# Performance work log

Hardware: AMD Instinct MI355X
Metric: run time of the kernel (lower is better)

The kernel has to match this reference:

```python
import jax, jax.numpy as jnp
import numpy as np

N_WIRES = 16
VAR_DEPTH = 2
BATCH = 16


def _param_sizes():
    sizes = []
    n = N_WIRES
    lay = 0
    while n > 1:
        sizes.append(4 * int(np.ceil(N_WIRES / 2 ** lay)) * VAR_DEPTH)
        n = (n + 1) // 2
        lay += 1
    return sizes  # [128, 64, 32, 16]


def _apply_1q(psi, gate, w):
    # psi: (B, 2, ..., 2); gate: (2,2) complex; wire w lives on axis w+1
    psi = jnp.moveaxis(psi, w + 1, -1)
    psi = jnp.einsum('...j,ij->...i', psi, gate)
    return jnp.moveaxis(psi, -1, w + 1)


def _rx(psi, th, w):
    c = jnp.cos(th / 2).astype(jnp.complex64)
    s = jnp.sin(th / 2).astype(jnp.complex64)
    gate = jnp.stack([jnp.stack([c, -1j * s]), jnp.stack([-1j * s, c])])
    return _apply_1q(psi, gate, w)


def _rz(psi, th, w):
    ph = jnp.exp(0.5j * th * jnp.array([-1.0, 1.0], jnp.float32)).astype(jnp.complex64)
    shape = [1] * psi.ndim
    shape[w + 1] = 2
    return psi * ph.reshape(shape)


def _rzz(psi, th, wa, wb):
    # diag(e^{-i t/2}, e^{i t/2}, e^{i t/2}, e^{-i t/2}) -> sign = -1 if bits equal else +1
    sgn = jnp.array([[-1.0, 1.0], [1.0, -1.0]], jnp.float32)
    ph = jnp.exp(0.5j * th * sgn).astype(jnp.complex64)  # symmetric, transpose-safe
    a, b = min(wa, wb) + 1, max(wa, wb) + 1
    shape = [1] * psi.ndim
    shape[a] = 2
    shape[b] = 2
    return psi * ph.reshape(shape)


def _cnot(psi, c, t):
    p0 = jax.lax.slice_in_dim(psi, 0, 1, axis=c + 1)
    p1 = jax.lax.slice_in_dim(psi, 1, 2, axis=c + 1)
    return jnp.concatenate([p0, jnp.flip(p1, axis=t + 1)], axis=c + 1)


def _conv_layer(psi, params, active):
    n = len(active)
    for d in range(VAR_DEPTH):
        for j in range(n):
            base = 4 * j + d * 4 * n
            psi = _rx(psi, params[base + 0], active[j])
            psi = _rz(psi, params[base + 1], active[j])
            psi = _rx(psi, params[base + 2], active[j])
        for bg in (0, 1):
            for j in range(bg, n, 2):
                jn = (j + 1) % n  # ring coupling (wraps last->first)
                base = 4 * j + d * 4 * n
                psi = _rzz(psi, params[base + 3], active[j], active[jn])
    return psi


def _pool(psi, active):
    for j in range(0, len(active), 2):
        if j + 1 < len(active):
            psi = _cnot(psi, active[j], active[j + 1])
    return psi, active[::2]


def _forward(psi, params_list):
    active = list(range(N_WIRES))
    for p in params_list:
        psi = _conv_layer(psi, p, active)
        if len(active) > 1:
            psi, active = _pool(psi, active)
    w = active[0]  # measure Z on the surviving wire (wire 0)
    prob = psi.real ** 2 + psi.imag ** 2
    axes = tuple(a for a in range(1, psi.ndim) if a != w + 1)
    p2 = prob.sum(axis=axes)  # (B, 2)
    return p2[:, 0] - p2[:, 1]


def setup_inputs() -> dict:
    key = jax.random.key(0)
    ks = jax.random.split(key, 8)
    dim = 2 ** N_WIRES
    x_re = jax.random.normal(ks[0], (BATCH, dim), dtype=jnp.float32)
    x_im = jax.random.normal(ks[1], (BATCH, dim), dtype=jnp.float32)
    nrm = jnp.sqrt(jnp.sum(x_re ** 2 + x_im ** 2, axis=1, keepdims=True))
    x_re = x_re / nrm
    x_im = x_im / nrm
    sizes = _param_sizes()
    two_pi = 2.0 * np.pi
    params = [jax.random.uniform(ks[2 + i], (sizes[i],), dtype=jnp.float32) * two_pi
              for i in range(len(sizes))]
    return {"x_re": x_re, "x_im": x_im,
            "params0": params[0], "params1": params[1],
            "params2": params[2], "params3": params[3]}


def reference(x_re, x_im, params0, params1, params2, params3):
    psi = (x_re + 1j * x_im).astype(jnp.complex64)
    psi = psi.reshape((BATCH,) + (2,) * N_WIRES)
    return _forward(psi, [params0, params1, params2, params3])
```

## Files before the change

### kernel.cpp

```cpp
#include <hip/hip_runtime.h>


#define DEV __device__ __forceinline__
#define TBL(i) (tbl + (i)*8)

__device__ static const unsigned char G_CP[60] = {
  15,14,13,12,11,10,9,8,7,6,5,4,3,2,1,0,
  15,14,13,12,11,10,9,8,7,6,5,4,3,2,1,0,
  15,13,11,9,7,5,3,1,
  15,13,11,9,7,5,3,1,
  15,11,7,3,
  15,11,7,3,
  15,7,
  15,7
};
__device__ static const unsigned char G_CQ[60] = {
  14,13,12,11,10,9,8,7,6,5,4,3,2,1,0,15,
  14,13,12,11,10,9,8,7,6,5,4,3,2,1,0,15,
  13,11,9,7,5,3,1,15,
  13,11,9,7,5,3,1,15,
  11,7,3,15,
  11,7,3,15,
  7,15,
  7,15
};

DEV float2 F2(float x, float y){ float2 r; r.x = x; r.y = y; return r; }
DEV float2 cmulf(float2 a, float2 b){ return F2(a.x*b.x - a.y*b.y, a.x*b.y + a.y*b.x); }
DEV int swz(int j){ return j ^ ((j>>4)&15) ^ ((j>>8)&15); }

template<int A,int B>
DEV int mapj(int t, int s){
  int j = ((s&1)<<A) | (((s>>1)&1)<<B);
  int ti = 0;
  #pragma unroll
  for (int b=0;b<11;b++){
    if (b!=A && b!=B){ j |= ((t>>ti)&1)<<b; ti++; }
  }
  return j;
}

template<int SB>
DEV void gate4(float2* a, const float* __restrict__ g){
  float u00r=g[0],u00i=g[1],u01r=g[2],u01i=g[3],u10r=g[4],u10i=g[5],u11r=g[6],u11i=g[7];
  #pragma unroll
  for (int m=0;m<2;m++){
    int i0 = (SB==0) ? (m<<1) : m;
    int i1 = i0 | (1<<SB);
    float2 x0=a[i0], x1=a[i1];
    a[i0] = F2(u00r*x0.x - u00i*x0.y + u01r*x1.x - u01i*x1.y,
               u00r*x0.y + u00i*x0.x + u01r*x1.y + u01i*x1.x);
    a[i1] = F2(u10r*x0.x - u10i*x0.y + u11r*x1.x - u11i*x1.y,
               u10r*x0.y + u10i*x0.x + u11r*x1.y + u11i*x1.x);
  }
}

template<int C0,int N,unsigned M0,unsigned M1>
DEV void diag4(float2* a, const float* __restrict__ tbl, unsigned Ib){
  const unsigned regmask = M0|M1;
  float2 F0 = F2(1.f, 0.f);
  #pragma unroll
  for (int k=0;k<N;k++){
    const int p = G_CP[C0+k], q = G_CQ[C0+k];
    if ( !(((1u<<p)|(1u<<q)) & regmask) ){
      float c = tbl[480 + 2*(C0+k)], s = tbl[481 + 2*(C0+k)];
      unsigned x = ((Ib>>p) ^ (Ib>>q)) & 1u;
      F0 = cmulf(F0, F2(c, x ? s : -s));
    }
  }
  #pragma unroll
  for (int r=0;r<4;r++){
    unsigned Ir = Ib ^ ((r&1)?M0:0u) ^ ((r&2)?M1:0u);
    float2 ph = F0;
    #pragma unroll
    for (int k=0;k<N;k++){
      const int p = G_CP[C0+k], q = G_CQ[C0+k];
      if ( ((1u<<p)|(1u<<q)) & regmask ){
        float c = tbl[480 + 2*(C0+k)], s = tbl[481 + 2*(C0+k)];
        unsigned x = ((Ir>>p) ^ (Ir>>q)) & 1u;
        ph = cmulf(ph, F2(c, x ? s : -s));
      }
    }
    a[r] = cmulf(a[r], ph);
  }
}

DEV unsigned Ia(int j, int o){ return (unsigned)(j | (o<<11)); }
DEV unsigned Ib2(int j, int o){ return (unsigned)((j&63) | (o<<6) | ((j>>6)<<11)); }
DEV unsigned Ic(int j, int o){
  return (unsigned)( ((j&1)<<1) | (((j>>1)&1)<<3) | (((j>>2)&1)<<5)
       | (((j>>3)&63)<<6) | (((j>>9)&1)<<13) | (((j>>10)&1)<<15)
       | (o&1) | (((o>>1)&1)<<2) | (((o>>2)&1)<<4) | (((o>>3)&1)<<12) | (((o>>4)&1)<<14) );
}
DEV int s2perm(int j){ return j ^ (((j>>8)&1)<<6) ^ (((j>>4)&1)<<2) ^ (((j>>1)&1)<<0); }
DEV int s3perm(int j){ return j ^ (((j>>10)&1)<<8) ^ (((j>>4)&1)<<1); }

__global__ void k_setup(const float* __restrict__ p0, const float* __restrict__ p1,
                        const float* __restrict__ p2, const float* __restrict__ p3,
                        float* __restrict__ tbl, float* __restrict__ out){
  int g = threadIdx.x;
  if (g < 16) out[g] = 0.f;
  if (g >= 60) return;
  int d, j, n; const float* P;
  if (g < 32)      { n=16; d=(g>>4)&1; j=g&15; P=p0; }
  else if (g < 48) { n=8;  d=(g>>3)&1; j=g&7;  P=p1; }
  else if (g < 56) { n=4;  d=(g>>2)&1; j=g&3;  P=p2; }
  else             { n=2;  d=(g>>1)&1; j=g&1;  P=p3; }
  int base = 4*j + 4*n*d;
  double th0 = P[base+0], th1 = P[base+1], th2 = P[base+2], th3 = P[base+3];
  double c0 = cos(th0*0.5), s0 = sin(th0*0.5);
  double ca = cos(th1*0.5), sa = sin(th1*0.5);
  double c2 = cos(th2*0.5), s2 = sin(th2*0.5);
  double B00r =  ca*c0, B00i = -sa*c0;
  double B01r = -sa*s0, B01i = -ca*s0;
  double B10r =  sa*s0, B10i = -ca*s0;
  double B11r =  ca*c0, B11i =  sa*c0;
  float* o = tbl + g*8;
  o[0]=(float)(c2*B00r + s2*B10i); o[1]=(float)(c2*B00i - s2*B10r);
  o[2]=(float)(c2*B01r + s2*B11i); o[3]=(float)(c2*B01i - s2*B11r);
  o[4]=(float)(s2*B00i + c2*B10r); o[5]=(float)(-s2*B00r + c2*B10i);
  o[6]=(float)(s2*B01i + c2*B11r); o[7]=(float)(-s2*B01r + c2*B11i);
  tbl[480 + 2*g] = (float)cos(th3*0.5);
  tbl[481 + 2*g] = (float)sin(th3*0.5);
}

__global__ __launch_bounds__(512, 4)
void k_p1(const float* __restrict__ xre, const float* __restrict__ xim,
          const float* __restrict__ tbl, float2* __restrict__ st){
  const int t = threadIdx.x;
  const int batch = blockIdx.x >> 5, o = blockIdx.x & 31;
  const unsigned hi = ((unsigned)batch<<16) | ((unsigned)o<<11);
  __shared__ float2 lds[2][2048];
  float2 a[4];
  {
    unsigned base = hi | ((unsigned)t<<2);
    float4 re = *(const float4*)(xre + base);
    float4 im = *(const float4*)(xim + base);
    a[0]=F2(re.x,im.x); a[1]=F2(re.y,im.y); a[2]=F2(re.z,im.z); a[3]=F2(re.w,im.w);
  }
  gate4<0>(a, TBL(15)); gate4<1>(a, TBL(14));
  #pragma unroll
  for (int s=0;s<4;s++) lds[0][swz(mapj<0,1>(t,s))] = a[s];
  __syncthreads();
  #pragma unroll
  for (int s=0;s<4;s++) a[s] = lds[0][swz(mapj<2,3>(t,s))];
  gate4<0>(a, TBL(13)); gate4<1>(a, TBL(12));
  #pragma unroll
  for (int s=0;s<4;s++) lds[1][swz(mapj<2,3>(t,s))] = a[s];
  __syncthreads();
  #pragma unroll
  for (int s=0;s<4;s++) a[s] = lds[1][swz(mapj<4,5>(t,s))];
  gate4<0>(a, TBL(11)); gate4<1>(a, TBL(10));
  #pragma unroll
  for (int s=0;s<4;s++) lds[0][swz(mapj<4,5>(t,s))] = a[s];
  __syncthreads();
  #pragma unroll
  for (int s=0;s<4;s++) a[s] = lds[0][swz(mapj<6,7>(t,s))];
  gate4<0>(a, TBL(9)); gate4<1>(a, TBL(8));
  #pragma unroll
  for (int s=0;s<4;s++) lds[1][swz(mapj<6,7>(t,s))] = a[s];
  __syncthreads();
  #pragma unroll
  for (int s=0;s<4;s++) a[s] = lds[1][swz(mapj<8,9>(t,s))];
  gate4<0>(a, TBL(7)); gate4<1>(a, TBL(6));
  #pragma unroll
  for (int s=0;s<4;s++) lds[0][swz(mapj<8,9>(t,s))] = a[s];
  __syncthreads();
  #pragma unroll
  for (int s=0;s<4;s++) a[s] = lds[0][swz(mapj<0,10>(t,s))];
  gate4<1>(a, TBL(5));
  #pragma unroll
  for (int s=0;s<4;s++) st[hi | (unsigned)mapj<0,10>(t,s)] = a[s];
}

__global__ __launch_bounds__(512, 4)
void k_p2(const float* __restrict__ tbl, float2* __restrict__ st){
  const int t = threadIdx.x;
  const int batch = blockIdx.x >> 5, o = blockIdx.x & 31;
  const unsigned bb = (unsigned)batch<<16;
  __shared__ float2 lds[2][2048];
  float2 a[4];
  #pragma unroll
  for (int s=0;s<4;s++) a[s] = st[bb | Ib2(mapj<10,9>(t,s), o)];
  gate4<0>(a, TBL(0)); gate4<1>(a, TBL(1));
  #pragma unroll
  for (int s=0;s<4;s++) lds[0][swz(mapj<10,9>(t,s))] = a[s];
  __syncthreads();
  #pragma unroll
  for (int s=0;s<4;s++) a[s] = lds[0][swz(mapj<8,7>(t,s))];
  gate4<0>(a, TBL(2)); gate4<1>(a, TBL(3));
  #pragma unroll
  for (int s=0;s<4;s++) lds[1][swz(mapj<8,7>(t,s))] = a[s];
  __syncthreads();
  #pragma unroll
  for (int s=0;s<4;s++) a[s] = lds[1][swz(mapj<6,5>(t,s))];
  gate4<0>(a, TBL(4));
  diag4<0,16, (1u<<11),(1u<<5)>(a, tbl, Ib2(mapj<6,5>(t,0), o));
  gate4<0>(a, TBL(20)); gate4<1>(a, TBL(26));
  #pragma unroll
  for (int s=0;s<4;s++) lds[0][swz(mapj<6,5>(t,s))] = a[s];
  __syncthreads();
  #pragma unroll
  for (int s=0;s<4;s++) a[s] = lds[0][swz(mapj<7,8>(t,s))];
  gate4<0>(a, TBL(19)); gate4<1>(a, TBL(18));
  #pragma unroll
  for (int s=0;s<4;s++) lds[1][swz(mapj<7,8>(t,s))] = a[s];
  __syncthreads();
  #pragma unroll
  for (int s=0;s<4;s++) a[s] = lds[1][swz(mapj<9,10>(t,s))];
  gate4<0>(a, TBL(17)); gate4<1>(a, TBL(16));
  #pragma unroll
  for (int s=0;s<4;s++) lds[0][swz(mapj<9,10>(t,s))] = a[s];
  __syncthreads();
  #pragma unroll
  for (int s=0;s<4;s++) a[s] = lds[0][swz(mapj<0,1>(t,s))];
  gate4<0>(a, TBL(31)); gate4<1>(a, TBL(30));
  #pragma unroll
  for (int s=0;s<4;s++) lds[1][swz(mapj<0,1>(t,s))] = a[s];
  __syncthreads();
  #pragma unroll
  for (int s=0;s<4;s++) a[s] = lds[1][swz(mapj<2,3>(t,s))];
  gate4<0>(a, TBL(29)); gate4<1>(a, TBL(28));
  #pragma unroll
  for (int s=0;s<4;s++) lds[0][swz(mapj<2,3>(t,s))] = a[s];
  __syncthreads();
  #pragma unroll
  for (int s=0;s<4;s++) a[s] = lds[0][swz(mapj<4,10>(t,s))];
  gate4<0>(a, TBL(27));
  #pragma unroll
  for (int s=0;s<4;s++) st[bb | Ib2(mapj<4,10>(t,s), o)] = a[s];
}

__global__ __launch_bounds__(512, 4)
void k_p3(const float* __restrict__ tbl, float2* __restrict__ st){
  const int t = threadIdx.x;
  const int batch = blockIdx.x >> 5, o = blockIdx.x & 31;
  const unsigned hi = ((unsigned)batch<<16) | ((unsigned)o<<11);
  __shared__ float2 lds[2][2048];
  float2 a[4];
  #pragma unroll
  for (int s=0;s<4;s++) a[s] = st[hi | (unsigned)mapj<6,7>(t,s)];
  gate4<0>(a, TBL(25)); gate4<1>(a, TBL(24));
  #pragma unroll
  for (int s=0;s<4;s++) lds[0][swz(mapj<6,7>(t,s))] = a[s];
  __syncthreads();
  #pragma unroll
  for (int s=0;s<4;s++) a[s] = lds[0][swz(mapj<8,9>(t,s))];
  gate4<0>(a, TBL(23)); gate4<1>(a, TBL(22));
  #pragma unroll
  for (int s=0;s<4;s++) lds[1][swz(mapj<8,9>(t,s))] = a[s];
  __syncthreads();
  #pragma unroll
  for (int s=0;s<4;s++) a[s] = lds[1][swz(mapj<0,10>(t,s))];
  gate4<1>(a, TBL(21));
  diag4<16,16, 1u,(1u<<10)>(a, tbl, Ia(mapj<0,10>(t,0), o));
  #pragma unroll
  for (int s=0;s<4;s++) st[hi | (unsigned)mapj<0,10>(t,s)] = a[s];
}

__global__ __launch_bounds__(512, 4)
void k_p4(const float* __restrict__ tbl, float2* __restrict__ st, float* __restrict__ out){
  const int t = threadIdx.x;
  const int batch = blockIdx.x >> 5, o = blockIdx.x & 31;
  const unsigned bb = (unsigned)batch<<16;
  __shared__ float2 lds[2][2048];
  __shared__ float red[8];
  float2 a[4];
  #pragma unroll
  for (int s=0;s<4;s++){
    unsigned I = Ic(mapj<10,9>(t,s), o);
    I ^= (I & 0xAAAAu) >> 1;
    a[s] = st[bb | I];
  }
  gate4<0>(a, TBL(32)); gate4<1>(a, TBL(33));
  #pragma unroll
  for (int s=0;s<4;s++) lds[0][swz(mapj<10,9>(t,s))] = a[s];
  __syncthreads();
  #pragma unroll
  for (int s=0;s<4;s++) a[s] = lds[0][swz(mapj<8,6>(t,s))];
  gate4<0>(a, TBL(34)); gate4<1>(a, TBL(35));
  #pragma unroll
  for (int s=0;s<4;s++) lds[1][swz(mapj<8,6>(t,s))] = a[s];
  __syncthreads();
  #pragma unroll
  for (int s=0;s<4;s++) a[s] = lds[1][swz(mapj<4,2>(t,s))];
  gate4<0>(a, TBL(36)); gate4<1>(a, TBL(37));
  #pragma unroll
  for (int s=0;s<4;s++) lds[0][swz(mapj<4,2>(t,s))] = a[s];
  __syncthreads();
  #pragma unroll
  for (int s=0;s<4;s++) a[s] = lds[0][swz(mapj<1,0>(t,s))];
  gate4<0>(a, TBL(38)); gate4<1>(a, TBL(39));
  diag4<32,8, (1u<<3),(1u<<1)>(a, tbl, Ic(mapj<1,0>(t,0), o));
  gate4<0>(a, TBL(46)); gate4<1>(a, TBL(47));
  #pragma unroll
  for (int s=0;s<4;s++) lds[1][swz(mapj<1,0>(t,s))] = a[s];
  __syncthreads();
  #pragma unroll
  for (int s=0;s<4;s++) a[s] = lds[1][swz(mapj<2,4>(t,s))];
  gate4<0>(a, TBL(45)); gate4<1>(a, TBL(44));
  #pragma unroll
  for (int s=0;s<4;s++) lds[0][swz(mapj<2,4>(t,s))] = a[s];
  __syncthreads();
  #pragma unroll
  for (int s=0;s<4;s++) a[s] = lds[0][swz(mapj<6,8>(t,s))];
  gate4<0>(a, TBL(43)); gate4<1>(a, TBL(42));
  #pragma unroll
  for (int s=0;s<4;s++) lds[1][swz(mapj<6,8>(t,s))] = a[s];
  __syncthreads();
  #pragma unroll
  for (int s=0;s<4;s++) a[s] = lds[1][swz(mapj<9,10>(t,s))];
  gate4<0>(a, TBL(41)); gate4<1>(a, TBL(40));
  diag4<40,8, (1u<<13),(1u<<15)>(a, tbl, Ic(mapj<9,10>(t,0), o));
  { float2 tmp=a[2]; a[2]=a[3]; a[3]=tmp; }
  gate4<1>(a, TBL(48));
  #pragma unroll
  for (int s=0;s<4;s++) lds[0][swz(mapj<9,10>(t,s))] = a[s];
  __syncthreads();
  #pragma unroll
  for (int s=0;s<4;s++) a[s] = lds[0][swz(s2perm(mapj<8,4>(t,s)))];
  gate4<0>(a, TBL(49)); gate4<1>(a, TBL(50));
  #pragma unroll
  for (int s=0;s<4;s++) lds[1][swz(mapj<8,4>(t,s))] = a[s];
  __syncthreads();
  #pragma unroll
  for (int s=0;s<4;s++) a[s] = lds[1][swz(mapj<1,10>(t,s))];
  gate4<0>(a, TBL(51));
  diag4<48,4, (1u<<3),(1u<<15)>(a, tbl, Ic(mapj<1,10>(t,0), o));
  gate4<0>(a, TBL(55)); gate4<1>(a, TBL(52));
  #pragma unroll
  for (int s=0;s<4;s++) lds[0][swz(mapj<1,10>(t,s))] = a[s];
  __syncthreads();
  #pragma unroll
  for (int s=0;s<4;s++) a[s] = lds[0][swz(mapj<4,8>(t,s))];
  gate4<0>(a, TBL(54)); gate4<1>(a, TBL(53));
  diag4<52,4, (1u<<7),(1u<<11)>(a, tbl, Ic(mapj<4,8>(t,0), o));
  #pragma unroll
  for (int s=0;s<4;s++) lds[1][swz(mapj<4,8>(t,s))] = a[s];
  __syncthreads();
  #pragma unroll
  for (int s=0;s<4;s++) a[s] = lds[1][swz(s3perm(mapj<4,10>(t,s)))];
  gate4<0>(a, TBL(57)); gate4<1>(a, TBL(56));
  diag4<56,2, (1u<<7),(1u<<15)>(a, tbl, Ic(mapj<4,10>(t,0), o));
  gate4<1>(a, TBL(58));
  float s = 0.f;
  #pragma unroll
  for (int r=0;r<4;r++){
    float w = a[r].x*a[r].x + a[r].y*a[r].y;
    s += (r & 2) ? -w : w;
  }
  #pragma unroll
  for (int off=32; off>0; off>>=1) s += __shfl_down(s, off);
  if ((t & 63) == 0) red[t>>6] = s;
  __syncthreads();
  if (t == 0){
    float tot = 0.f;
    #pragma unroll
    for (int w=0; w<8; w++) tot += red[w];
    atomicAdd(out + batch, tot);
  }
}

extern "C" void kernel_launch(void* const* d_in, const int* in_sizes, int n_in,
                              void* d_out, int out_size, void* d_ws, size_t ws_size,
                              hipStream_t stream) {
  const float* xre = (const float*)d_in[0];
  const float* xim = (const float*)d_in[1];
  const float* p0  = (const float*)d_in[2];
  const float* p1  = (const float*)d_in[3];
  const float* p2  = (const float*)d_in[4];
  const float* p3  = (const float*)d_in[5];
  float* out = (float*)d_out;
  float2* st = (float2*)d_ws;
  float* tbl = (float*)((char*)d_ws + (8u<<20));

  k_setup<<<1, 64, 0, stream>>>(p0, p1, p2, p3, tbl, out);
  k_p1<<<512, 512, 0, stream>>>(xre, xim, tbl, st);
  k_p2<<<512, 512, 0, stream>>>(tbl, st);
  k_p3<<<512, 512, 0, stream>>>(tbl, st);
  k_p4<<<512, 512, 0, stream>>>(tbl, st, out);
}
```

Measured before the change: 114.3 us.

## Fuse setup and stage-3 kernels into neighbours, build gate table per block in LDS

Removes the separate setup kernel by having every block recompute the gate-parameter table into shared memory. It also folds the stage-3 gates and their ring diagonal into the final kernel through a new index mapping. This cuts two kernel launches and one full round trip of the state vector through global memory. In exchange, each block redundantly runs double-precision trig for 60 threads, and the last kernel becomes longer with more barriers.

```diff
diff --git a/kernel.cpp b/kernel.cpp
--- a/kernel.cpp
+++ b/kernel.cpp
@@ -2,7 +2,7 @@
 
 
 #define DEV __device__ __forceinline__
-#define TBL(i) (tbl + (i)*8)
+#define TB(i) (tbs + (i)*8)
 
 __device__ static const unsigned char G_CP[60] = {
   15,14,13,12,11,10,9,8,7,6,5,4,3,2,1,0,
@@ -41,7 +41,7 @@
 }
 
 template<int SB>
-DEV void gate4(float2* a, const float* __restrict__ g){
+DEV void gate4(float2* a, const float* g){
   float u00r=g[0],u00i=g[1],u01r=g[2],u01i=g[3],u10r=g[4],u10i=g[5],u11r=g[6],u11i=g[7];
   #pragma unroll
   for (int m=0;m<2;m++){
@@ -56,14 +56,14 @@
 }
 
 template<int C0,int N,unsigned M0,unsigned M1>
-DEV void diag4(float2* a, const float* __restrict__ tbl, unsigned Ib){
+DEV void diag4(float2* a, const float* tbs, unsigned Ib){
   const unsigned regmask = M0|M1;
   float2 F0 = F2(1.f, 0.f);
   #pragma unroll
   for (int k=0;k<N;k++){
     const int p = G_CP[C0+k], q = G_CQ[C0+k];
     if ( !(((1u<<p)|(1u<<q)) & regmask) ){
-      float c = tbl[480 + 2*(C0+k)], s = tbl[481 + 2*(C0+k)];
+      float c = tbs[480 + 2*(C0+k)], s = tbs[481 + 2*(C0+k)];
       unsigned x = ((Ib>>p) ^ (Ib>>q)) & 1u;
       F0 = cmulf(F0, F2(c, x ? s : -s));
     }
@@ -76,7 +76,7 @@
     for (int k=0;k<N;k++){
       const int p = G_CP[C0+k], q = G_CQ[C0+k];
       if ( ((1u<<p)|(1u<<q)) & regmask ){
-        float c = tbl[480 + 2*(C0+k)], s = tbl[481 + 2*(C0+k)];
+        float c = tbs[480 + 2*(C0+k)], s = tbs[481 + 2*(C0+k)];
         unsigned x = ((Ir>>p) ^ (Ir>>q)) & 1u;
         ph = cmulf(ph, F2(c, x ? s : -s));
       }
@@ -92,257 +92,263 @@
        | (((j>>3)&63)<<6) | (((j>>9)&1)<<13) | (((j>>10)&1)<<15)
        | (o&1) | (((o>>1)&1)<<2) | (((o>>2)&1)<<4) | (((o>>3)&1)<<12) | (((o>>4)&1)<<14) );
 }
+DEV unsigned s1b(unsigned I){ return I ^ ((I & 0xA02Au) >> 1); }
+DEV int s1aperm(int j){ return j ^ (((j>>8)&1)<<7) ^ (((j>>6)&1)<<5) ^ (((j>>4)&1)<<3); }
 DEV int s2perm(int j){ return j ^ (((j>>8)&1)<<6) ^ (((j>>4)&1)<<2) ^ (((j>>1)&1)<<0); }
 DEV int s3perm(int j){ return j ^ (((j>>10)&1)<<8) ^ (((j>>4)&1)<<1); }
 
-__global__ void k_setup(const float* __restrict__ p0, const float* __restrict__ p1,
-                        const float* __restrict__ p2, const float* __restrict__ p3,
-                        float* __restrict__ tbl, float* __restrict__ out){
-  int g = threadIdx.x;
-  if (g < 16) out[g] = 0.f;
-  if (g >= 60) return;
-  int d, j, n; const float* P;
-  if (g < 32)      { n=16; d=(g>>4)&1; j=g&15; P=p0; }
-  else if (g < 48) { n=8;  d=(g>>3)&1; j=g&7;  P=p1; }
-  else if (g < 56) { n=4;  d=(g>>2)&1; j=g&3;  P=p2; }
-  else             { n=2;  d=(g>>1)&1; j=g&1;  P=p3; }
-  int base = 4*j + 4*n*d;
-  double th0 = P[base+0], th1 = P[base+1], th2 = P[base+2], th3 = P[base+3];
-  double c0 = cos(th0*0.5), s0 = sin(th0*0.5);
-  double ca = cos(th1*0.5), sa = sin(th1*0.5);
-  double c2 = cos(th2*0.5), s2 = sin(th2*0.5);
-  double B00r =  ca*c0, B00i = -sa*c0;
-  double B01r = -sa*s0, B01i = -ca*s0;
-  double B10r =  sa*s0, B10i = -ca*s0;
-  double B11r =  ca*c0, B11i =  sa*c0;
-  float* o = tbl + g*8;
-  o[0]=(float)(c2*B00r + s2*B10i); o[1]=(float)(c2*B00i - s2*B10r);
-  o[2]=(float)(c2*B01r + s2*B11i); o[3]=(float)(c2*B01i - s2*B11r);
-  o[4]=(float)(s2*B00i + c2*B10r); o[5]=(float)(-s2*B00r + c2*B10i);
-  o[6]=(float)(s2*B01i + c2*B11r); o[7]=(float)(-s2*B01r + c2*B11i);
-  tbl[480 + 2*g] = (float)cos(th3*0.5);
-  tbl[481 + 2*g] = (float)sin(th3*0.5);
+DEV void build_tbl(int t, const float* __restrict__ p0, const float* __restrict__ p1,
+                   const float* __restrict__ p2, const float* __restrict__ p3,
+                   float* tbs){
+  if (t < 60){
+    int g = t;
+    int d, j, n; const float* P;
+    if (g < 32)      { n=16; d=(g>>4)&1; j=g&15; P=p0; }
+    else if (g < 48) { n=8;  d=(g>>3)&1; j=g&7;  P=p1; }
+    else if (g < 56) { n=4;  d=(g>>2)&1; j=g&3;  P=p2; }
+    else             { n=2;  d=(g>>1)&1; j=g&1;  P=p3; }
+    int base = 4*j + 4*n*d;
+    double th0 = P[base+0], th1 = P[base+1], th2 = P[base+2], th3 = P[base+3];
+    double c0 = cos(th0*0.5), s0 = sin(th0*0.5);
+    double ca = cos(th1*0.5), sa = sin(th1*0.5);
+    double c2 = cos(th2*0.5), s2 = sin(th2*0.5);
+    double B00r =  ca*c0, B00i = -sa*c0;
+    double B01r = -sa*s0, B01i = -ca*s0;
+    double B10r =  sa*s0, B10i = -ca*s0;
+    double B11r =  ca*c0, B11i =  sa*c0;
+    float* oo = tbs + g*8;
+    oo[0]=(float)(c2*B00r + s2*B10i); oo[1]=(float)(c2*B00i - s2*B10r);
+    oo[2]=(float)(c2*B01r + s2*B11i); oo[3]=(float)(c2*B01i - s2*B11r);
+    oo[4]=(float)(s2*B00i + c2*B10r); oo[5]=(float)(-s2*B00r + c2*B10i);
+    oo[6]=(float)(s2*B01i + c2*B11r); oo[7]=(float)(-s2*B01r + c2*B11i);
+    tbs[480 + 2*g] = (float)cos(th3*0.5);
+    tbs[481 + 2*g] = (float)sin(th3*0.5);
+  }
 }
 
 __global__ __launch_bounds__(512, 4)
 void k_p1(const float* __restrict__ xre, const float* __restrict__ xim,
-          const float* __restrict__ tbl, float2* __restrict__ st){
+          const float* __restrict__ p0, const float* __restrict__ p1,
+          const float* __restrict__ p2, const float* __restrict__ p3,
+          float2* __restrict__ st, float* __restrict__ out){
   const int t = threadIdx.x;
   const int batch = blockIdx.x >> 5, o = blockIdx.x & 31;
   const unsigned hi = ((unsigned)batch<<16) | ((unsigned)o<<11);
   __shared__ float2 lds[2][2048];
+  __shared__ float tbs[600];
   float2 a[4];
+  if (blockIdx.x == 0 && t < 16) out[t] = 0.f;
+  build_tbl(t, p0, p1, p2, p3, tbs);
+  __syncthreads();
   {
     unsigned base = hi | ((unsigned)t<<2);
     float4 re = *(const float4*)(xre + base);
     float4 im = *(const float4*)(xim + base);
     a[0]=F2(re.x,im.x); a[1]=F2(re.y,im.y); a[2]=F2(re.z,im.z); a[3]=F2(re.w,im.w);
   }
-  gate4<0>(a, TBL(15)); gate4<1>(a, TBL(14));
+  gate4<0>(a, TB(15)); gate4<1>(a, TB(14));
   #pragma unroll
   for (int s=0;s<4;s++) lds[0][swz(mapj<0,1>(t,s))] = a[s];
   __syncthreads();
   #pragma unroll
   for (int s=0;s<4;s++) a[s] = lds[0][swz(mapj<2,3>(t,s))];
-  gate4<0>(a, TBL(13)); gate4<1>(a, TBL(12));
+  gate4<0>(a, TB(13)); gate4<1>(a, TB(12));
   #pragma unroll
   for (int s=0;s<4;s++) lds[1][swz(mapj<2,3>(t,s))] = a[s];
   __syncthreads();
   #pragma unroll
   for (int s=0;s<4;s++) a[s] = lds[1][swz(mapj<4,5>(t,s))];
-  gate4<0>(a, TBL(11)); gate4<1>(a, TBL(10));
+  gate4<0>(a, TB(11)); gate4<1>(a, TB(10));
   #pragma unroll
   for (int s=0;s<4;s++) lds[0][swz(mapj<4,5>(t,s))] = a[s];
   __syncthreads();
   #pragma unroll
   for (int s=0;s<4;s++) a[s] = lds[0][swz(mapj<6,7>(t,s))];
-  gate4<0>(a, TBL(9)); gate4<1>(a, TBL(8));
+  gate4<0>(a, TB(9)); gate4<1>(a, TB(8));
   #pragma unroll
   for (int s=0;s<4;s++) lds[1][swz(mapj<6,7>(t,s))] = a[s];
   __syncthreads();
   #pragma unroll
   for (int s=0;s<4;s++) a[s] = lds[1][swz(mapj<8,9>(t,s))];
-  gate4<0>(a, TBL(7)); gate4<1>(a, TBL(6));
+  gate4<0>(a, TB(7)); gate4<1>(a, TB(6));
   #pragma unroll
   for (int s=0;s<4;s++) lds[0][swz(mapj<8,9>(t,s))] = a[s];
   __syncthreads();
   #pragma unroll
   for (int s=0;s<4;s++) a[s] = lds[0][swz(mapj<0,10>(t,s))];
-  gate4<1>(a, TBL(5));
+  gate4<1>(a, TB(5));
   #pragma unroll
   for (int s=0;s<4;s++) st[hi | (unsigned)mapj<0,10>(t,s)] = a[s];
 }
 
 __global__ __launch_bounds__(512, 4)
-void k_p2(const float* __restrict__ tbl, float2* __restrict__ st){
+void k_p2(const float* __restrict__ p0, const float* __restrict__ p1,
+          const float* __restrict__ p2, const float* __restrict__ p3,
+          float2* __restrict__ st){
   const int t = threadIdx.x;
   const int batch = blockIdx.x >> 5, o = blockIdx.x & 31;
   const unsigned bb = (unsigned)batch<<16;
   __shared__ float2 lds[2][2048];
+  __shared__ float tbs[600];
   float2 a[4];
+  build_tbl(t, p0, p1, p2, p3, tbs);
+  __syncthreads();
   #pragma unroll
   for (int s=0;s<4;s++) a[s] = st[bb | Ib2(mapj<10,9>(t,s), o)];
-  gate4<0>(a, TBL(0)); gate4<1>(a, TBL(1));
+  gate4<0>(a, TB(0)); gate4<1>(a, TB(1));
   #pragma unroll
   for (int s=0;s<4;s++) lds[0][swz(mapj<10,9>(t,s))] = a[s];
   __syncthreads();
   #pragma unroll
   for (int s=0;s<4;s++) a[s] = lds[0][swz(mapj<8,7>(t,s))];
-  gate4<0>(a, TBL(2)); gate4<1>(a, TBL(3));
+  gate4<0>(a, TB(2)); gate4<1>(a, TB(3));
   #pragma unroll
   for (int s=0;s<4;s++) lds[1][swz(mapj<8,7>(t,s))] = a[s];
   __syncthreads();
   #pragma unroll
   for (int s=0;s<4;s++) a[s] = lds[1][swz(mapj<6,5>(t,s))];
-  gate4<0>(a, TBL(4));
-  diag4<0,16, (1u<<11),(1u<<5)>(a, tbl, Ib2(mapj<6,5>(t,0), o));
-  gate4<0>(a, TBL(20)); gate4<1>(a, TBL(26));
+  gate4<0>(a, TB(4));
+  diag4<0,16, (1u<<11),(1u<<5)>(a, tbs, Ib2(mapj<6,5>(t,0), o));
+  gate4<0>(a, TB(20)); gate4<1>(a, TB(26));
   #pragma unroll
   for (int s=0;s<4;s++) lds[0][swz(mapj<6,5>(t,s))] = a[s];
   __syncthreads();
   #pragma unroll
   for (int s=0;s<4;s++) a[s] = lds[0][swz(mapj<7,8>(t,s))];
-  gate4<0>(a, TBL(19)); gate4<1>(a, TBL(18));
+  gate4<0>(a, TB(19)); gate4<1>(a, TB(18));
   #pragma unroll
   for (int s=0;s<4;s++) lds[1][swz(mapj<7,8>(t,s))] = a[s];
   __syncthreads();
   #pragma unroll
   for (int s=0;s<4;s++) a[s] = lds[1][swz(mapj<9,10>(t,s))];
-  gate4<0>(a, TBL(17)); gate4<1>(a, TBL(16));
+  gate4<0>(a, TB(17)); gate4<1>(a, TB(16));
   #pragma unroll
   for (int s=0;s<4;s++) lds[0][swz(mapj<9,10>(t,s))] = a[s];
   __syncthreads();
   #pragma unroll
   for (int s=0;s<4;s++) a[s] = lds[0][swz(mapj<0,1>(t,s))];
-  gate4<0>(a, TBL(31)); gate4<1>(a, TBL(30));
+  gate4<0>(a, TB(31)); gate4<1>(a, TB(30));
   #pragma unroll
   for (int s=0;s<4;s++) lds[1][swz(mapj<0,1>(t,s))] = a[s];
   __syncthreads();
   #pragma unroll
   for (int s=0;s<4;s++) a[s] = lds[1][swz(mapj<2,3>(t,s))];
-  gate4<0>(a, TBL(29)); gate4<1>(a, TBL(28));
+  gate4<0>(a, TB(29)); gate4<1>(a, TB(28));
   #pragma unroll
   for (int s=0;s<4;s++) lds[0][swz(mapj<2,3>(t,s))] = a[s];
   __syncthreads();
   #pragma unroll
   for (int s=0;s<4;s++) a[s] = lds[0][swz(mapj<4,10>(t,s))];
-  gate4<0>(a, TBL(27));
+  gate4<0>(a, TB(27));
   #pragma unroll
   for (int s=0;s<4;s++) st[bb | Ib2(mapj<4,10>(t,s), o)] = a[s];
 }
 
 __global__ __launch_bounds__(512, 4)
-void k_p3(const float* __restrict__ tbl, float2* __restrict__ st){
-  const int t = threadIdx.x;
-  const int batch = blockIdx.x >> 5, o = blockIdx.x & 31;
-  const unsigned hi = ((unsigned)batch<<16) | ((unsigned)o<<11);
-  __shared__ float2 lds[2][2048];
-  float2 a[4];
-  #pragma unroll
-  for (int s=0;s<4;s++) a[s] = st[hi | (unsigned)mapj<6,7>(t,s)];
-  gate4<0>(a, TBL(25)); gate4<1>(a, TBL(24));
-  #pragma unroll
-  for (int s=0;s<4;s++) lds[0][swz(mapj<6,7>(t,s))] = a[s];
-  __syncthreads();
-  #pragma unroll
-  for (int s=0;s<4;s++) a[s] = lds[0][swz(mapj<8,9>(t,s))];
-  gate4<0>(a, TBL(23)); gate4<1>(a, TBL(22));
-  #pragma unroll
-  for (int s=0;s<4;s++) lds[1][swz(mapj<8,9>(t,s))] = a[s];
-  __syncthreads();
-  #pragma unroll
-  for (int s=0;s<4;s++) a[s] = lds[1][swz(mapj<0,10>(t,s))];
-  gate4<1>(a, TBL(21));
-  diag4<16,16, 1u,(1u<<10)>(a, tbl, Ia(mapj<0,10>(t,0), o));
-  #pragma unroll
-  for (int s=0;s<4;s++) st[hi | (unsigned)mapj<0,10>(t,s)] = a[s];
-}
-
-__global__ __launch_bounds__(512, 4)
-void k_p4(const float* __restrict__ tbl, float2* __restrict__ st, float* __restrict__ out){
+void k_p4(const float* __restrict__ p0, const float* __restrict__ p1,
+          const float* __restrict__ p2, const float* __restrict__ p3,
+          float2* __restrict__ st, float* __restrict__ out){
   const int t = threadIdx.x;
   const int batch = blockIdx.x >> 5, o = blockIdx.x & 31;
   const unsigned bb = (unsigned)batch<<16;
   __shared__ float2 lds[2][2048];
+  __shared__ float tbs[600];
   __shared__ float red[8];
   float2 a[4];
-  #pragma unroll
-  for (int s=0;s<4;s++){
-    unsigned I = Ic(mapj<10,9>(t,s), o);
-    I ^= (I & 0xAAAAu) >> 1;
-    a[s] = st[bb | I];
-  }
-  gate4<0>(a, TBL(32)); gate4<1>(a, TBL(33));
-  #pragma unroll
-  for (int s=0;s<4;s++) lds[0][swz(mapj<10,9>(t,s))] = a[s];
-  __syncthreads();
-  #pragma unroll
-  for (int s=0;s<4;s++) a[s] = lds[0][swz(mapj<8,6>(t,s))];
-  gate4<0>(a, TBL(34)); gate4<1>(a, TBL(35));
-  #pragma unroll
-  for (int s=0;s<4;s++) lds[1][swz(mapj<8,6>(t,s))] = a[s];
-  __syncthreads();
-  #pragma unroll
-  for (int s=0;s<4;s++) a[s] = lds[1][swz(mapj<4,2>(t,s))];
-  gate4<0>(a, TBL(36)); gate4<1>(a, TBL(37));
-  #pragma unroll
-  for (int s=0;s<4;s++) lds[0][swz(mapj<4,2>(t,s))] = a[s];
-  __syncthreads();
-  #pragma unroll
-  for (int s=0;s<4;s++) a[s] = lds[0][swz(mapj<1,0>(t,s))];
-  gate4<0>(a, TBL(38)); gate4<1>(a, TBL(39));
-  diag4<32,8, (1u<<3),(1u<<1)>(a, tbl, Ic(mapj<1,0>(t,0), o));
-  gate4<0>(a, TBL(46)); gate4<1>(a, TBL(47));
-  #pragma unroll
-  for (int s=0;s<4;s++) lds[1][swz(mapj<1,0>(t,s))] = a[s];
-  __syncthreads();
-  #pragma unroll
-  for (int s=0;s<4;s++) a[s] = lds[1][swz(mapj<2,4>(t,s))];
-  gate4<0>(a, TBL(45)); gate4<1>(a, TBL(44));
-  #pragma unroll
-  for (int s=0;s<4;s++) lds[0][swz(mapj<2,4>(t,s))] = a[s];
-  __syncthreads();
-  #pragma unroll
-  for (int s=0;s<4;s++) a[s] = lds[0][swz(mapj<6,8>(t,s))];
-  gate4<0>(a, TBL(43)); gate4<1>(a, TBL(42));
-  #pragma unroll
-  for (int s=0;s<4;s++) lds[1][swz(mapj<6,8>(t,s))] = a[s];
-  __syncthreads();
-  #pragma unroll
-  for (int s=0;s<4;s++) a[s] = lds[1][swz(mapj<9,10>(t,s))];
-  gate4<0>(a, TBL(41)); gate4<1>(a, TBL(40));
-  diag4<40,8, (1u<<13),(1u<<15)>(a, tbl, Ic(mapj<9,10>(t,0), o));
+  build_tbl(t, p0, p1, p2, p3, tbs);
+  __syncthreads();
+  #pragma unroll
+  for (int s=0;s<4;s++) a[s] = st[bb | s1b(Ic(mapj<3,4>(t,s), o))];
+  gate4<0>(a, TB(25)); gate4<1>(a, TB(24));
+  #pragma unroll
+  for (int s=0;s<4;s++) lds[0][swz(mapj<3,4>(t,s))] = a[s];
+  __syncthreads();
+  #pragma unroll
+  for (int s=0;s<4;s++) a[s] = lds[0][swz(mapj<5,6>(t,s))];
+  gate4<0>(a, TB(23)); gate4<1>(a, TB(22));
+  #pragma unroll
+  for (int s=0;s<4;s++) lds[1][swz(mapj<5,6>(t,s))] = a[s];
+  __syncthreads();
+  #pragma unroll
+  for (int s=0;s<4;s++) a[s] = lds[1][swz(mapj<7,8>(t,s))];
+  gate4<0>(a, TB(21));
+  diag4<16,16, (1u<<10),(1u<<11)>(a, tbs, s1b(Ic(mapj<7,8>(t,0), o)));
+  #pragma unroll
+  for (int s=0;s<4;s++) lds[0][swz(mapj<7,8>(t,s))] = a[s];
+  __syncthreads();
+  #pragma unroll
+  for (int s=0;s<4;s++) a[s] = lds[0][swz(s1aperm(mapj<10,9>(t,s)))];
+  gate4<0>(a, TB(32)); gate4<1>(a, TB(33));
+  #pragma unroll
+  for (int s=0;s<4;s++) lds[1][swz(mapj<10,9>(t,s))] = a[s];
+  __syncthreads();
+  #pragma unroll
+  for (int s=0;s<4;s++) a[s] = lds[1][swz(mapj<8,6>(t,s))];
+  gate4<0>(a, TB(34)); gate4<1>(a, TB(35));
+  #pragma unroll
+  for (int s=0;s<4;s++) lds[0][swz(mapj<8,6>(t,s))] = a[s];
+  __syncthreads();
+  #pragma unroll
+  for (int s=0;s<4;s++) a[s] = lds[0][swz(mapj<4,2>(t,s))];
+  gate4<0>(a, TB(36)); gate4<1>(a, TB(37));
+  #pragma unroll
+  for (int s=0;s<4;s++) lds[1][swz(mapj<4,2>(t,s))] = a[s];
+  __syncthreads();
+  #pragma unroll
+  for (int s=0;s<4;s++) a[s] = lds[1][swz(mapj<1,0>(t,s))];
+  gate4<0>(a, TB(38)); gate4<1>(a, TB(39));
+  diag4<32,8, (1u<<3),(1u<<1)>(a, tbs, Ic(mapj<1,0>(t,0), o));
+  gate4<0>(a, TB(46)); gate4<1>(a, TB(47));
+  #pragma unroll
+  for (int s=0;s<4;s++) lds[0][swz(mapj<1,0>(t,s))] = a[s];
+  __syncthreads();
+  #pragma unroll
+  for (int s=0;s<4;s++) a[s] = lds[0][swz(mapj<2,4>(t,s))];
+  gate4<0>(a, TB(45)); gate4<1>(a, TB(44));
+  #pragma unroll
+  for (int s=0;s<4;s++) lds[1][swz(mapj<2,4>(t,s))] = a[s];
+  __syncthreads();
+  #pragma unroll
+  for (int s=0;s<4;s++) a[s] = lds[1][swz(mapj<6,8>(t,s))];
+  gate4<0>(a, TB(43)); gate4<1>(a, TB(42));
+  #pragma unroll
+  for (int s=0;s<4;s++) lds[0][swz(mapj<6,8>(t,s))] = a[s];
+  __syncthreads();
+  #pragma unroll
+  for (int s=0;s<4;s++) a[s] = lds[0][swz(mapj<9,10>(t,s))];
+  gate4<0>(a, TB(41)); gate4<1>(a, TB(40));
+  diag4<40,8, (1u<<13),(1u<<15)>(a, tbs, Ic(mapj<9,10>(t,0), o));
   { float2 tmp=a[2]; a[2]=a[3]; a[3]=tmp; }
-  gate4<1>(a, TBL(48));
-  #pragma unroll
-  for (int s=0;s<4;s++) lds[0][swz(mapj<9,10>(t,s))] = a[s];
-  __syncthreads();
-  #pragma unroll
-  for (int s=0;s<4;s++) a[s] = lds[0][swz(s2perm(mapj<8,4>(t,s)))];
-  gate4<0>(a, TBL(49)); gate4<1>(a, TBL(50));
-  #pragma unroll
-  for (int s=0;s<4;s++) lds[1][swz(mapj<8,4>(t,s))] = a[s];
-  __syncthreads();
-  #pragma unroll
-  for (int s=0;s<4;s++) a[s] = lds[1][swz(mapj<1,10>(t,s))];
-  gate4<0>(a, TBL(51));
-  diag4<48,4, (1u<<3),(1u<<15)>(a, tbl, Ic(mapj<1,10>(t,0), o));
-  gate4<0>(a, TBL(55)); gate4<1>(a, TBL(52));
-  #pragma unroll
-  for (int s=0;s<4;s++) lds[0][swz(mapj<1,10>(t,s))] = a[s];
-  __syncthreads();
-  #pragma unroll
-  for (int s=0;s<4;s++) a[s] = lds[0][swz(mapj<4,8>(t,s))];
-  gate4<0>(a, TBL(54)); gate4<1>(a, TBL(53));
-  diag4<52,4, (1u<<7),(1u<<11)>(a, tbl, Ic(mapj<4,8>(t,0), o));
-  #pragma unroll
-  for (int s=0;s<4;s++) lds[1][swz(mapj<4,8>(t,s))] = a[s];
-  __syncthreads();
-  #pragma unroll
-  for (int s=0;s<4;s++) a[s] = lds[1][swz(s3perm(mapj<4,10>(t,s)))];
-  gate4<0>(a, TBL(57)); gate4<1>(a, TBL(56));
-  diag4<56,2, (1u<<7),(1u<<15)>(a, tbl, Ic(mapj<4,10>(t,0), o));
-  gate4<1>(a, TBL(58));
+  gate4<1>(a, TB(48));
+  #pragma unroll
+  for (int s=0;s<4;s++) lds[1][swz(mapj<9,10>(t,s))] = a[s];
+  __syncthreads();
+  #pragma unroll
+  for (int s=0;s<4;s++) a[s] = lds[1][swz(s2perm(mapj<8,4>(t,s)))];
+  gate4<0>(a, TB(49)); gate4<1>(a, TB(50));
+  #pragma unroll
+  for (int s=0;s<4;s++) lds[0][swz(mapj<8,4>(t,s))] = a[s];
+  __syncthreads();
+  #pragma unroll
+  for (int s=0;s<4;s++) a[s] = lds[0][swz(mapj<1,10>(t,s))];
+  gate4<0>(a, TB(51));
+  diag4<48,4, (1u<<3),(1u<<15)>(a, tbs, Ic(mapj<1,10>(t,0), o));
+  gate4<0>(a, TB(55)); gate4<1>(a, TB(52));
+  #pragma unroll
+  for (int s=0;s<4;s++) lds[1][swz(mapj<1,10>(t,s))] = a[s];
+  __syncthreads();
+  #pragma unroll
+  for (int s=0;s<4;s++) a[s] = lds[1][swz(mapj<4,8>(t,s))];
+  gate4<0>(a, TB(54)); gate4<1>(a, TB(53));
+  diag4<52,4, (1u<<7),(1u<<11)>(a, tbs, Ic(mapj<4,8>(t,0), o));
+  #pragma unroll
+  for (int s=0;s<4;s++) lds[0][swz(mapj<4,8>(t,s))] = a[s];
+  __syncthreads();
+  #pragma unroll
+  for (int s=0;s<4;s++) a[s] = lds[0][swz(s3perm(mapj<4,10>(t,s)))];
+  gate4<0>(a, TB(57)); gate4<1>(a, TB(56));
+  diag4<56,2, (1u<<7),(1u<<15)>(a, tbs, Ic(mapj<4,10>(t,0), o));
+  gate4<1>(a, TB(58));
   float s = 0.f;
   #pragma unroll
   for (int r=0;r<4;r++){
@@ -372,11 +378,8 @@
   const float* p3  = (const float*)d_in[5];
   float* out = (float*)d_out;
   float2* st = (float2*)d_ws;
-  float* tbl = (float*)((char*)d_ws + (8u<<20));
-
-  k_setup<<<1, 64, 0, stream>>>(p0, p1, p2, p3, tbl, out);
-  k_p1<<<512, 512, 0, stream>>>(xre, xim, tbl, st);
-  k_p2<<<512, 512, 0, stream>>>(tbl, st);
-  k_p3<<<512, 512, 0, stream>>>(tbl, st);
-  k_p4<<<512, 512, 0, stream>>>(tbl, st, out);
-}
+
+  k_p1<<<512, 512, 0, stream>>>(xre, xim, p0, p1, p2, p3, st, out);
+  k_p2<<<512, 512, 0, stream>>>(p0, p1, p2, p3, st);
+  k_p4<<<512, 512, 0, stream>>>(p0, p1, p2, p3, st, out);
+}
```

After: 114.6 us. About the same (+0.3%).

## Fold third pass into final kernel and vectorize first-pass stores

Applied to the files above, without the earlier changes.

Removes the k_p3 kernel and performs its gates and RZZ diagonal at the start of k_p4, with index remapping (s1b, s1aperm) so the state loaded into k_p4 matches the permuted layout. This removes one full global read/write round trip of the 8 MB state and one kernel launch. k_p1 now writes its results as two float4 stores instead of four scattered float2 stores. Launch bounds are raised to 8 blocks per CU. The risk is extra register pressure and more LDS barriers in the longer k_p4.

```diff
diff --git a/kernel.cpp b/kernel.cpp
--- a/kernel.cpp
+++ b/kernel.cpp
@@ -92,6 +92,8 @@
        | (((j>>3)&63)<<6) | (((j>>9)&1)<<13) | (((j>>10)&1)<<15)
        | (o&1) | (((o>>1)&1)<<2) | (((o>>2)&1)<<4) | (((o>>3)&1)<<12) | (((o>>4)&1)<<14) );
 }
+DEV unsigned s1b(unsigned I){ return I ^ ((I & 0xA02Au) >> 1); }
+DEV int s1aperm(int j){ return j ^ (((j>>8)&1)<<7) ^ (((j>>6)&1)<<5) ^ (((j>>4)&1)<<3); }
 DEV int s2perm(int j){ return j ^ (((j>>8)&1)<<6) ^ (((j>>4)&1)<<2) ^ (((j>>1)&1)<<0); }
 DEV int s3perm(int j){ return j ^ (((j>>10)&1)<<8) ^ (((j>>4)&1)<<1); }
 
@@ -124,7 +126,7 @@
   tbl[481 + 2*g] = (float)sin(th3*0.5);
 }
 
-__global__ __launch_bounds__(512, 4)
+__global__ __launch_bounds__(512, 8)
 void k_p1(const float* __restrict__ xre, const float* __restrict__ xim,
           const float* __restrict__ tbl, float2* __restrict__ st){
   const int t = threadIdx.x;
@@ -169,11 +171,16 @@
   #pragma unroll
   for (int s=0;s<4;s++) a[s] = lds[0][swz(mapj<0,10>(t,s))];
   gate4<1>(a, TBL(5));
-  #pragma unroll
-  for (int s=0;s<4;s++) st[hi | (unsigned)mapj<0,10>(t,s)] = a[s];
-}
-
-__global__ __launch_bounds__(512, 4)
+  {
+    unsigned jb = hi | ((unsigned)t<<1);
+    float4 v0; v0.x=a[0].x; v0.y=a[0].y; v0.z=a[1].x; v0.w=a[1].y;
+    float4 v1; v1.x=a[2].x; v1.y=a[2].y; v1.z=a[3].x; v1.w=a[3].y;
+    *(float4*)(st + jb) = v0;
+    *(float4*)(st + jb + 1024) = v1;
+  }
+}
+
+__global__ __launch_bounds__(512, 8)
 void k_p2(const float* __restrict__ tbl, float2* __restrict__ st){
   const int t = threadIdx.x;
   const int batch = blockIdx.x >> 5, o = blockIdx.x & 31;
@@ -231,34 +238,7 @@
   for (int s=0;s<4;s++) st[bb | Ib2(mapj<4,10>(t,s), o)] = a[s];
 }
 
-__global__ __launch_bounds__(512, 4)
-void k_p3(const float* __restrict__ tbl, float2* __restrict__ st){
-  const int t = threadIdx.x;
-  const int batch = blockIdx.x >> 5, o = blockIdx.x & 31;
-  const unsigned hi = ((unsigned)batch<<16) | ((unsigned)o<<11);
-  __shared__ float2 lds[2][2048];
-  float2 a[4];
-  #pragma unroll
-  for (int s=0;s<4;s++) a[s] = st[hi | (unsigned)mapj<6,7>(t,s)];
-  gate4<0>(a, TBL(25)); gate4<1>(a, TBL(24));
-  #pragma unroll
-  for (int s=0;s<4;s++) lds[0][swz(mapj<6,7>(t,s))] = a[s];
-  __syncthreads();
-  #pragma unroll
-  for (int s=0;s<4;s++) a[s] = lds[0][swz(mapj<8,9>(t,s))];
-  gate4<0>(a, TBL(23)); gate4<1>(a, TBL(22));
-  #pragma unroll
-  for (int s=0;s<4;s++) lds[1][swz(mapj<8,9>(t,s))] = a[s];
-  __syncthreads();
-  #pragma unroll
-  for (int s=0;s<4;s++) a[s] = lds[1][swz(mapj<0,10>(t,s))];
-  gate4<1>(a, TBL(21));
-  diag4<16,16, 1u,(1u<<10)>(a, tbl, Ia(mapj<0,10>(t,0), o));
-  #pragma unroll
-  for (int s=0;s<4;s++) st[hi | (unsigned)mapj<0,10>(t,s)] = a[s];
-}
-
-__global__ __launch_bounds__(512, 4)
+__global__ __launch_bounds__(512, 8)
 void k_p4(const float* __restrict__ tbl, float2* __restrict__ st, float* __restrict__ out){
   const int t = threadIdx.x;
   const int batch = blockIdx.x >> 5, o = blockIdx.x & 31;
@@ -267,79 +247,94 @@
   __shared__ float red[8];
   float2 a[4];
   #pragma unroll
-  for (int s=0;s<4;s++){
-    unsigned I = Ic(mapj<10,9>(t,s), o);
-    I ^= (I & 0xAAAAu) >> 1;
-    a[s] = st[bb | I];
-  }
+  for (int s=0;s<4;s++) a[s] = st[bb | s1b(Ic(mapj<3,4>(t,s), o))];
+  gate4<0>(a, TBL(25)); gate4<1>(a, TBL(24));
+  #pragma unroll
+  for (int s=0;s<4;s++) lds[0][swz(mapj<3,4>(t,s))] = a[s];
+  __syncthreads();
+  #pragma unroll
+  for (int s=0;s<4;s++) a[s] = lds[0][swz(mapj<5,6>(t,s))];
+  gate4<0>(a, TBL(23)); gate4<1>(a, TBL(22));
+  #pragma unroll
+  for (int s=0;s<4;s++) lds[1][swz(mapj<5,6>(t,s))] = a[s];
+  __syncthreads();
+  #pragma unroll
+  for (int s=0;s<4;s++) a[s] = lds[1][swz(mapj<7,8>(t,s))];
+  gate4<0>(a, TBL(21));
+  diag4<16,16, (1u<<10),(1u<<11)>(a, tbl, s1b(Ic(mapj<7,8>(t,0), o)));
+  #pragma unroll
+  for (int s=0;s<4;s++) lds[0][swz(mapj<7,8>(t,s))] = a[s];
+  __syncthreads();
+  #pragma unroll
+  for (int s=0;s<4;s++) a[s] = lds[0][swz(s1aperm(mapj<10,9>(t,s)))];
   gate4<0>(a, TBL(32)); gate4<1>(a, TBL(33));
   #pragma unroll
-  for (int s=0;s<4;s++) lds[0][swz(mapj<10,9>(t,s))] = a[s];
-  __syncthreads();
-  #pragma unroll
-  for (int s=0;s<4;s++) a[s] = lds[0][swz(mapj<8,6>(t,s))];
+  for (int s=0;s<4;s++) lds[1][swz(mapj<10,9>(t,s))] = a[s];
+  __syncthreads();
+  #pragma unroll
+  for (int s=0;s<4;s++) a[s] = lds[1][swz(mapj<8,6>(t,s))];
   gate4<0>(a, TBL(34)); gate4<1>(a, TBL(35));
   #pragma unroll
-  for (int s=0;s<4;s++) lds[1][swz(mapj<8,6>(t,s))] = a[s];
-  __syncthreads();
-  #pragma unroll
-  for (int s=0;s<4;s++) a[s] = lds[1][swz(mapj<4,2>(t,s))];
+  for (int s=0;s<4;s++) lds[0][swz(mapj<8,6>(t,s))] = a[s];
+  __syncthreads();
+  #pragma unroll
+  for (int s=0;s<4;s++) a[s] = lds[0][swz(mapj<4,2>(t,s))];
   gate4<0>(a, TBL(36)); gate4<1>(a, TBL(37));
   #pragma unroll
-  for (int s=0;s<4;s++) lds[0][swz(mapj<4,2>(t,s))] = a[s];
-  __syncthreads();
-  #pragma unroll
-  for (int s=0;s<4;s++) a[s] = lds[0][swz(mapj<1,0>(t,s))];
+  for (int s=0;s<4;s++) lds[1][swz(mapj<4,2>(t,s))] = a[s];
+  __syncthreads();
+  #pragma unroll
+  for (int s=0;s<4;s++) a[s] = lds[1][swz(mapj<1,0>(t,s))];
   gate4<0>(a, TBL(38)); gate4<1>(a, TBL(39));
   diag4<32,8, (1u<<3),(1u<<1)>(a, tbl, Ic(mapj<1,0>(t,0), o));
   gate4<0>(a, TBL(46)); gate4<1>(a, TBL(47));
   #pragma unroll
-  for (int s=0;s<4;s++) lds[1][swz(mapj<1,0>(t,s))] = a[s];
-  __syncthreads();
-  #pragma unroll
-  for (int s=0;s<4;s++) a[s] = lds[1][swz(mapj<2,4>(t,s))];
+  for (int s=0;s<4;s++) lds[0][swz(mapj<1,0>(t,s))] = a[s];
+  __syncthreads();
+  #pragma unroll
+  for (int s=0;s<4;s++) a[s] = lds[0][swz(mapj<2,4>(t,s))];
   gate4<0>(a, TBL(45)); gate4<1>(a, TBL(44));
   #pragma unroll
-  for (int s=0;s<4;s++) lds[0][swz(mapj<2,4>(t,s))] = a[s];
-  __syncthreads();
-  #pragma unroll
-  for (int s=0;s<4;s++) a[s] = lds[0][swz(mapj<6,8>(t,s))];
+  for (int s=0;s<4;s++) lds[1][swz(mapj<2,4>(t,s))] = a[s];
+  __syncthreads();
+  #pragma unroll
+  for (int s=0;s<4;s++) a[s] = lds[1][swz(mapj<6,8>(t,s))];
   gate4<0>(a, TBL(43)); gate4<1>(a, TBL(42));
   #pragma unroll
-  for (int s=0;s<4;s++) lds[1][swz(mapj<6,8>(t,s))] = a[s];
-  __syncthreads();
-  #pragma unroll
-  for (int s=0;s<4;s++) a[s] = lds[1][swz(mapj<9,10>(t,s))];
+  for (int s=0;s<4;s++) lds[0][swz(mapj<6,8>(t,s))] = a[s];
+  __syncthreads();
+  #pragma unroll
+  for (int s=0;s<4;s++) a[s] = lds[0][swz(mapj<9,10>(t,s))];
   gate4<0>(a, TBL(41)); gate4<1>(a, TBL(40));
   diag4<40,8, (1u<<13),(1u<<15)>(a, tbl, Ic(mapj<9,10>(t,0), o));
   { float2 tmp=a[2]; a[2]=a[3]; a[3]=tmp; }
   gate4<1>(a, TBL(48));
   #pragma unroll
-  for (int s=0;s<4;s++) lds[0][swz(mapj<9,10>(t,s))] = a[s];
-  __syncthreads();
-  #pragma unroll
-  for (int s=0;s<4;s++) a[s] = lds[0][swz(s2perm(mapj<8,4>(t,s)))];
+  for (int s=0;s<4;s++) lds[1][swz(mapj<9,10>(t,s))] = a[s];
+  __syncthreads();
+  #pragma unroll
+  for (int s=0;s<4;s++) a[s] = lds[1][swz(s2perm(mapj<8,4>(t,s)))];
   gate4<0>(a, TBL(49)); gate4<1>(a, TBL(50));
   #pragma unroll
-  for (int s=0;s<4;s++) lds[1][swz(mapj<8,4>(t,s))] = a[s];
-  __syncthreads();
-  #pragma unroll
-  for (int s=0;s<4;s++) a[s] = lds[1][swz(mapj<1,10>(t,s))];
+  for (int s=0;s<4;s++) lds[0][swz(mapj<8,4>(t,s))] = a[s];
+  __syncthreads();
+  #pragma unroll
+  for (int s=0;s<4;s++) a[s] = lds[0][swz(mapj<1,10>(t,s))];
   gate4<0>(a, TBL(51));
   diag4<48,4, (1u<<3),(1u<<15)>(a, tbl, Ic(mapj<1,10>(t,0), o));
   gate4<0>(a, TBL(55)); gate4<1>(a, TBL(52));
   #pragma unroll
-  for (int s=0;s<4;s++) lds[0][swz(mapj<1,10>(t,s))] = a[s];
-  __syncthreads();
-  #pragma unroll
-  for (int s=0;s<4;s++) a[s] = lds[0][swz(mapj<4,8>(t,s))];
+  for (int s=0;s<4;s++) lds[1][swz(mapj<1,10>(t,s))] = a[s];
+  __syncthreads();
+  #pragma unroll
+  for (int s=0;s<4;s++) a[s] = lds[1][swz(mapj<4,8>(t,s))];
   gate4<0>(a, TBL(54)); gate4<1>(a, TBL(53));
   diag4<52,4, (1u<<7),(1u<<11)>(a, tbl, Ic(mapj<4,8>(t,0), o));
   #pragma unroll
-  for (int s=0;s<4;s++) lds[1][swz(mapj<4,8>(t,s))] = a[s];
-  __syncthreads();
-  #pragma unroll
-  for (int s=0;s<4;s++) a[s] = lds[1][swz(s3perm(mapj<4,10>(t,s)))];
+  for (int s=0;s<4;s++) lds[0][swz(mapj<4,8>(t,s))] = a[s];
+  __syncthreads();
+  #pragma unroll
+  for (int s=0;s<4;s++) a[s] = lds[0][swz(s3perm(mapj<4,10>(t,s)))];
   gate4<0>(a, TBL(57)); gate4<1>(a, TBL(56));
   diag4<56,2, (1u<<7),(1u<<15)>(a, tbl, Ic(mapj<4,10>(t,0), o));
   gate4<1>(a, TBL(58));
@@ -377,6 +372,5 @@
   k_setup<<<1, 64, 0, stream>>>(p0, p1, p2, p3, tbl, out);
   k_p1<<<512, 512, 0, stream>>>(xre, xim, tbl, st);
   k_p2<<<512, 512, 0, stream>>>(tbl, st);
-  k_p3<<<512, 512, 0, stream>>>(tbl, st);
   k_p4<<<512, 512, 0, stream>>>(tbl, st, out);
 }
```

Result: no change. 114.7 us (+0.4%).
